# Kernel tuning notes

Measured on AMD Instinct MI355X. Metric: run time of the kernel, lower is better.

Reference implementation:

```python
import jax, jax.numpy as jnp
import numpy as np

TOK_DIM = 512
POS_DIM = 512
N_HEADS = 16
HEAD_DIM = 64
D_MODEL = 1024
INNER = N_HEADS * HEAD_DIM
B, T = 4, 2048


def setup_inputs() -> dict:
    key = jax.random.key(0)
    ks = jax.random.split(key, 5)
    s = 0.02
    return {
        "x": jax.random.normal(ks[0], (B, T, TOK_DIM + POS_DIM), dtype=jnp.float32),
        "Wq": jax.random.normal(ks[1], (POS_DIM, INNER), dtype=jnp.float32) * s,
        "Wk": jax.random.normal(ks[2], (POS_DIM, INNER), dtype=jnp.float32) * s,
        "Wv": jax.random.normal(ks[3], (TOK_DIM, INNER), dtype=jnp.float32) * s,
        "Wo": jax.random.normal(ks[4], (INNER, D_MODEL), dtype=jnp.float32) * s,
    }


def reference(x, Wq, Wk, Wv, Wo):
    b, t, _ = x.shape
    x_tok = x[:, :, :TOK_DIM]
    x_pos = x[:, :, TOK_DIM:]
    # project and split heads: [B, H, T, Dh]
    q = (x_pos @ Wq).reshape(b, t, N_HEADS, HEAD_DIM).transpose(0, 2, 1, 3)
    k = (x_pos @ Wk).reshape(b, t, N_HEADS, HEAD_DIM).transpose(0, 2, 1, 3)
    v = (x_tok @ Wv).reshape(b, t, N_HEADS, HEAD_DIM).transpose(0, 2, 1, 3)
    att = jnp.einsum("bhqd,bhkd->bhqk", q, k) / jnp.sqrt(jnp.float32(HEAD_DIM))
    causal = jnp.tril(jnp.ones((t, t), dtype=bool))
    att = jnp.where(causal, att, -jnp.inf)
    att = jax.nn.softmax(att, axis=-1)
    out = jnp.einsum("bhqk,bhkd->bhqd", att, v)
    out = out.transpose(0, 2, 1, 3).reshape(b, t, INNER)
    return out @ Wo
```

## Files before the change

kernel.cpp:

```cpp
#include <hip/hip_runtime.h>
#include <stdint.h>


typedef unsigned short u16;
typedef __bf16 bf16;
typedef bf16 bf16x8 __attribute__((ext_vector_type(8)));
typedef u16 u16x8 __attribute__((ext_vector_type(8)));
typedef u16 u16x4 __attribute__((ext_vector_type(4)));
typedef float f32x4 __attribute__((ext_vector_type(4)));
typedef uint32_t u32x4 __attribute__((ext_vector_type(4)));

__device__ __forceinline__ u16 cvt_bf16(float f) {
  uint32_t u = __builtin_bit_cast(uint32_t, f);
  u += 0x7FFFu + ((u >> 16) & 1u);
  return (u16)(u >> 16);
}

__device__ __forceinline__ f32x4 mfma_bf(bf16x8 a, bf16x8 b, f32x4 c) {
  return __builtin_amdgcn_mfma_f32_16x16x32_bf16(a, b, c, 0, 0, 0);
}

typedef __attribute__((address_space(1))) const uint32_t g_u32;
typedef __attribute__((address_space(3))) uint32_t l_u32;
__device__ __forceinline__ void gload16(const u16* g, u16* l) {
  __builtin_amdgcn_global_load_lds((g_u32*)g, (l_u32*)l, 16, 0, 0);
}

__global__ __launch_bounds__(256) void prep(
    const float* __restrict__ x, const float* __restrict__ Wq,
    const float* __restrict__ Wk, const float* __restrict__ Wv,
    const float* __restrict__ Wo, u16* __restrict__ xtok,
    u16* __restrict__ xpos, u16* __restrict__ Wt, u16* __restrict__ WoT) {
  const int gid = blockIdx.x;
  const int tid = threadIdx.x;
  if (gid < 1024) {
    const int z = gid >> 8;
    const float* src = (z == 0) ? Wq : (z == 1) ? Wk : (z == 2) ? Wv : Wo;
    const int K = (z == 3) ? 1024 : 512;
    u16* dst = (z == 3) ? WoT : (Wt + (size_t)z * 1024 * 512);
    const int k0 = ((gid >> 4) & 15) * 64, n0 = (gid & 15) * 64;
    if (k0 >= K) return;
    __shared__ u16 T[64][68];
    const int r = tid >> 4, c = (tid & 15) * 4;
#pragma unroll
    for (int i = 0; i < 4; i++) {
      float4 v = *(const float4*)(src + (size_t)(k0 + r + i * 16) * 1024 + n0 + c);
      u16x4 b = {cvt_bf16(v.x), cvt_bf16(v.y), cvt_bf16(v.z), cvt_bf16(v.w)};
      *(u16x4*)&T[r + i * 16][c] = b;
    }
    __syncthreads();
#pragma unroll
    for (int i = 0; i < 4; i++) {
      int n = r + i * 16;
      u16x4 v;
#pragma unroll
      for (int j = 0; j < 4; j++) v[j] = T[c + j][n];
      *(u16x4*)(dst + (size_t)(n0 + n) * K + k0 + c) = v;
    }
  } else {
    int idx = (gid - 1024) * 256 + tid;
    int row = idx >> 8;
    int c4 = (idx & 255) * 4;
    float4 v = *(const float4*)(x + (size_t)row * 1024 + c4);
    u16x4 b = {cvt_bf16(v.x), cvt_bf16(v.y), cvt_bf16(v.z), cvt_bf16(v.w)};
    u16* dst = (c4 < 512) ? (xtok + (size_t)row * 512 + c4)
                          : (xpos + (size_t)row * 512 + c4 - 512);
    *(u16x4*)dst = b;
  }
}


#define YLD(P) {                                                             \
  const u16* pa_ = rA + (P)*4096;                                            \
  af[0] = *(const bf16x8*)(pa_ + 0*512 + colx);                              \
  af[1] = *(const bf16x8*)(pa_ + 1*512 + colx);                              \
  af[2] = *(const bf16x8*)(pa_ + 2*512 + colx);                              \
  af[3] = *(const bf16x8*)(pa_ + 3*512 + colx);                              \
  const u16* pb_ = rB + (P)*4096;                                            \
  bf[0] = *(const bf16x8*)(pb_ + 0*512 + colx);                              \
  bf[1] = *(const bf16x8*)(pb_ + 1*512 + colx);                              \
  bf[2] = *(const bf16x8*)(pb_ + 2*512 + colx);                              \
  bf[3] = *(const bf16x8*)(pb_ + 3*512 + colx); }

#define YMM {                                                                \
  acc[0][0] = mfma_bf(af[0], bf[0], acc[0][0]);                              \
  acc[0][1] = mfma_bf(af[0], bf[1], acc[0][1]);                              \
  acc[0][2] = mfma_bf(af[0], bf[2], acc[0][2]);                              \
  acc[0][3] = mfma_bf(af[0], bf[3], acc[0][3]);                              \
  acc[1][0] = mfma_bf(af[1], bf[0], acc[1][0]);                              \
  acc[1][1] = mfma_bf(af[1], bf[1], acc[1][1]);                              \
  acc[1][2] = mfma_bf(af[1], bf[2], acc[1][2]);                              \
  acc[1][3] = mfma_bf(af[1], bf[3], acc[1][3]);                              \
  acc[2][0] = mfma_bf(af[2], bf[0], acc[2][0]);                              \
  acc[2][1] = mfma_bf(af[2], bf[1], acc[2][1]);                              \
  acc[2][2] = mfma_bf(af[2], bf[2], acc[2][2]);                              \
  acc[2][3] = mfma_bf(af[2], bf[3], acc[2][3]);                              \
  acc[3][0] = mfma_bf(af[3], bf[0], acc[3][0]);                              \
  acc[3][1] = mfma_bf(af[3], bf[1], acc[3][1]);                              \
  acc[3][2] = mfma_bf(af[3], bf[2], acc[3][2]);                              \
  acc[3][3] = mfma_bf(af[3], bf[3], acc[3][3]); }

#define YST(P, KT) {                                                         \
  gload16(gA + (KT)*32, lA + (P)*4096);                                      \
  gload16(gA + (size_t)64*Kd + (KT)*32, lA + (P)*4096 + 2048);               \
  gload16(gB + (KT)*32, lB + (P)*4096);                                      \
  gload16(gB + (size_t)64*Kd + (KT)*32, lB + (P)*4096 + 2048); }

#define YPH_MID  asm volatile("" ::: "memory"); __builtin_amdgcn_s_barrier();\
  asm volatile("s_waitcnt lgkmcnt(0)" ::: "memory");                         \
  __builtin_amdgcn_s_setprio(1);

#define YPH_END  __builtin_amdgcn_s_setprio(0);                              \
  asm volatile("s_waitcnt vmcnt(4)" ::: "memory");                           \
  asm volatile("" ::: "memory"); __builtin_amdgcn_s_barrier();

template <int Kd>
__device__ __forceinline__ void gemm128_core(
    const u16* __restrict__ Aptr, const u16* __restrict__ Bptr,
    int m0, int n0, u16* smem, f32x4 (&acc)[4][4]) {
  constexpr int NKT = Kd / 32;
  const int tid = threadIdx.x;
  const int lane = tid & 63;
  const int mrow = lane & 15, quad = lane >> 4;
  const int w = tid >> 6, wm = w >> 1, wn = w & 1;

  u16* As = smem;
  u16* Bs = smem + 12288;

  const int lrs = tid >> 2, sp4 = tid & 3;
  const int slog = sp4 ^ (lrs & 3);
  const u16* gA = Aptr + (size_t)(m0 + lrs) * Kd + slog * 8;
  const u16* gB = Bptr + (size_t)(n0 + lrs) * Kd + slog * 8;
  u16* lA = As + tid * 8;
  u16* lB = Bs + tid * 8;

  const int colx = ((quad ^ (mrow & 3)) * 8);
  const u16* rA = As + (wm * 64 + mrow) * 32;
  const u16* rB = Bs + (wn * 64 + mrow) * 32;

  bf16x8 af[4], bf[4];

  YST(0, 0) YST(1, 1)
  asm volatile("s_waitcnt vmcnt(4)" ::: "memory");
  asm volatile("" ::: "memory");
  __builtin_amdgcn_s_barrier();

  int p = 0, ps = 2;
  for (int t = 0; t < NKT; ++t) {
    const int kt = (t + 2 < NKT) ? t + 2 : NKT - 1;
    YLD(p)
    YST(ps, kt)
    YPH_MID
    YMM
    YPH_END
    p = (p == 2) ? 0 : p + 1;
    ps = (ps == 2) ? 0 : ps + 1;
  }
  asm volatile("s_waitcnt vmcnt(0)" ::: "memory");
  __builtin_amdgcn_s_barrier();
}

__device__ __forceinline__ void xcd_remap(int& bx, int& by) {
  int flat = blockIdx.x + 8 * blockIdx.y;
  int wg = (flat & 7) * 64 + (flat >> 3);
  bx = wg & 7;
  by = wg >> 3;
}

__global__ __launch_bounds__(256, 3) void gemm_qkv128(
    const u16* __restrict__ xtok, const u16* __restrict__ xpos,
    const u16* __restrict__ Wt, u16* __restrict__ qkv,
    u16* __restrict__ vperm) {
  const int z = blockIdx.z;
  const u16* A = (z == 2) ? xtok : xpos;
  const u16* Bt = Wt + (size_t)z * 1024 * 512;
  u16* outp = qkv + (size_t)z * (64u * 2048u * 64u);
  const float osc = (z == 0) ? 0.18033688011112042f : 1.0f;
  int bx, by;
  xcd_remap(bx, by);
  const int m0 = by * 128, n0 = bx * 128;

  __shared__ __align__(16) u16 smem[24576];
  f32x4 acc[4][4];
#pragma unroll
  for (int i = 0; i < 4; i++)
#pragma unroll
    for (int j = 0; j < 4; j++) acc[i][j] = (f32x4){0.f, 0.f, 0.f, 0.f};

  gemm128_core<512>(A, Bt, m0, n0, smem, acc);

  const int tid = threadIdx.x;
  const int lane = tid & 63;
  const int mrow = lane & 15, quad = lane >> 4;
  const int w = tid >> 6, wm = w >> 1, wn = w & 1;

  if (z != 2) {
#pragma unroll
    for (int mi = 0; mi < 4; mi++)
#pragma unroll
      for (int ni = 0; ni < 4; ni++)
#pragma unroll
        for (int r = 0; r < 4; r++) {
          int m = m0 + wm * 64 + mi * 16 + quad * 4 + r;
          int n = n0 + wn * 64 + ni * 16 + mrow;
          int bb = m >> 11, t = m & 2047;
          int h = n >> 6, d = n & 63;
          outp[(((size_t)(bb * 16 + h)) * 2048 + t) * 64 + d] =
              cvt_bf16(acc[mi][ni][r] * osc);
        }
  } else {
#pragma unroll
    for (int mi = 0; mi < 4; mi++)
#pragma unroll
      for (int ni = 0; ni < 4; ni++)
#pragma unroll
        for (int r = 0; r < 4; r++) {
          int m = m0 + wm * 64 + mi * 16 + quad * 4 + r;
          int n = n0 + wn * 64 + ni * 16 + mrow;
          int bb = m >> 11, t = m & 2047;
          int h = n >> 6, d = n & 63;
          int k6 = t & 63;
          int pos = (k6 & 32) + ((k6 >> 4) & 1) * 4 + ((k6 >> 2) & 3) * 8 +
                    (k6 & 3);
          vperm[(((size_t)(bb * 16 + h)) * 64 + d) * 2048 + (t & ~63) + pos] =
              cvt_bf16(acc[mi][ni][r]);
        }
  }
}

__global__ __launch_bounds__(256, 3) void gemm_out128(
    const u16* __restrict__ Am, const u16* __restrict__ WoT,
    float* __restrict__ out) {
  int bx, by;
  xcd_remap(bx, by);
  const int m0 = by * 128, n0 = bx * 128;

  __shared__ __align__(16) u16 smem[24576];
  f32x4 acc[4][4];
#pragma unroll
  for (int i = 0; i < 4; i++)
#pragma unroll
    for (int j = 0; j < 4; j++) acc[i][j] = (f32x4){0.f, 0.f, 0.f, 0.f};

  gemm128_core<1024>(Am, WoT, m0, n0, smem, acc);

  const int tid = threadIdx.x;
  const int lane = tid & 63;
  const int mrow = lane & 15, quad = lane >> 4;
  const int w = tid >> 6, wm = w >> 1, wn = w & 1;

#pragma unroll
  for (int mi = 0; mi < 4; mi++)
#pragma unroll
    for (int ni = 0; ni < 4; ni++)
#pragma unroll
      for (int r = 0; r < 4; r++) {
        int m = m0 + wm * 64 + mi * 16 + quad * 4 + r;
        int n = n0 + wn * 64 + ni * 16 + mrow;
        out[(size_t)m * 1024 + n] = acc[mi][ni][r];
      }
}

__global__ __launch_bounds__(256, 3) void attn(
    const u16* __restrict__ qkv, const u16* __restrict__ vperm,
    u16* __restrict__ aout) {
  const int bh = blockIdx.x;
  const int qt = 15 - blockIdx.y;
  const int bb = bh >> 4, h = bh & 15;
  const u16* Qp = qkv + (size_t)bh * (2048 * 64);
  const u16* Kp = qkv + (size_t)(64 + bh) * (2048 * 64);
  const u16* Vp = vperm + (size_t)bh * (64 * 2048);

  __shared__ __align__(16) u16 smem[2][4][64 * 32];

  const int tid = threadIdx.x;
  const int lane = tid & 63;
  const int w = tid >> 6;
  const int mrow = lane & 15;
  const int quad = lane >> 4;
  const int srow = w * 16 + (lane >> 2);
  const int sc = (lane & 3) * 8;
  const int soff = srow * 32 + sc;

  const u16x8 onesu = {0x3F80, 0x3F80, 0x3F80, 0x3F80,
                       0x3F80, 0x3F80, 0x3F80, 0x3F80};
  const bf16x8 ones = __builtin_bit_cast(bf16x8, onesu);

  const u16* kgb = Kp + (size_t)srow * 64 + sc;
  const u16* vgb = Vp + (size_t)srow * 2048 + sc;

  const int q0 = qt * 128;
  const int nk = 2 * qt + 2;
  const int qw = q0 + w * 32;

  const u16* qbase = Qp + (size_t)(qw + mrow) * 64 + quad * 8;
  const bf16x8 qf00 = *(const bf16x8*)qbase;
  const bf16x8 qf01 = *(const bf16x8*)(qbase + 32);
  const bf16x8 qf10 = *(const bf16x8*)(qbase + 16 * 64);
  const bf16x8 qf11 = *(const bf16x8*)(qbase + 16 * 64 + 32);

  f32x4 o[2][4], ol[2];
#pragma unroll
  for (int g = 0; g < 2; ++g) {
#pragma unroll
    for (int dt = 0; dt < 4; ++dt) o[g][dt] = (f32x4){0.f, 0.f, 0.f, 0.f};
    ol[g] = (f32x4){0.f, 0.f, 0.f, 0.f};
  }

  u16x8 ka0 = *(const u16x8*)kgb;
  u16x8 ka1 = *(const u16x8*)(kgb + 32);
  u16x8 va0 = *(const u16x8*)vgb;
  u16x8 va1 = *(const u16x8*)(vgb + 32);

  for (int it = 0; it < nk; ++it) {
    u16* buf = &smem[it & 1][0][0];
    *(u16x8*)(buf + 0 * 2048 + soff) = ka0;
    *(u16x8*)(buf + 1 * 2048 + soff) = ka1;
    *(u16x8*)(buf + 2 * 2048 + soff) = va0;
    *(u16x8*)(buf + 3 * 2048 + soff) = va1;

    if (it + 1 < nk) {
      const int kn = (it + 1) * 64;
      ka0 = *(const u16x8*)(kgb + (size_t)kn * 64);
      ka1 = *(const u16x8*)(kgb + (size_t)kn * 64 + 32);
      va0 = *(const u16x8*)(vgb + kn);
      va1 = *(const u16x8*)(vgb + kn + 32);
    }

    __syncthreads();

    const int k0 = it * 64;
    if (k0 > qw + 31) continue;

    f32x4 s[2][4];
#pragma unroll
    for (int nt = 0; nt < 4; ++nt) {
      bf16x8 kf0 = *(const bf16x8*)(buf + 0 * 2048 + (nt * 16 + mrow) * 32 + quad * 8);
      bf16x8 kf1 = *(const bf16x8*)(buf + 1 * 2048 + (nt * 16 + mrow) * 32 + quad * 8);
      f32x4 z0 = (f32x4){0.f, 0.f, 0.f, 0.f};
      z0 = mfma_bf(kf0, qf00, z0);
      s[0][nt] = mfma_bf(kf1, qf01, z0);
      f32x4 z1 = (f32x4){0.f, 0.f, 0.f, 0.f};
      z1 = mfma_bf(kf0, qf10, z1);
      s[1][nt] = mfma_bf(kf1, qf11, z1);
    }

    if (k0 + 63 > qw) {
#pragma unroll
      for (int g = 0; g < 2; ++g)
#pragma unroll
        for (int nt = 0; nt < 4; ++nt)
#pragma unroll
          for (int r = 0; r < 4; ++r)
            if (k0 + nt * 16 + quad * 4 + r > qw + g * 16 + mrow)
              s[g][nt][r] = -1e30f;
    }
#pragma unroll
    for (int g = 0; g < 2; ++g)
#pragma unroll
      for (int nt = 0; nt < 4; ++nt)
#pragma unroll
        for (int r = 0; r < 4; ++r)
          s[g][nt][r] = __builtin_amdgcn_exp2f(s[g][nt][r]);

    bf16x8 pf[2][2];
#pragma unroll
    for (int g = 0; g < 2; ++g) {
      pf[g][0] = (bf16x8){(bf16)s[g][0][0], (bf16)s[g][0][1],
                          (bf16)s[g][0][2], (bf16)s[g][0][3],
                          (bf16)s[g][1][0], (bf16)s[g][1][1],
                          (bf16)s[g][1][2], (bf16)s[g][1][3]};
      pf[g][1] = (bf16x8){(bf16)s[g][2][0], (bf16)s[g][2][1],
                          (bf16)s[g][2][2], (bf16)s[g][2][3],
                          (bf16)s[g][3][0], (bf16)s[g][3][1],
                          (bf16)s[g][3][2], (bf16)s[g][3][3]};
      ol[g] = mfma_bf(ones, pf[g][0], ol[g]);
      ol[g] = mfma_bf(ones, pf[g][1], ol[g]);
    }

#pragma unroll
    for (int dt = 0; dt < 4; ++dt) {
      bf16x8 vf0 = *(const bf16x8*)(buf + 2 * 2048 + (dt * 16 + mrow) * 32 + quad * 8);
      bf16x8 vf1 = *(const bf16x8*)(buf + 3 * 2048 + (dt * 16 + mrow) * 32 + quad * 8);
      o[0][dt] = mfma_bf(vf0, pf[0][0], o[0][dt]);
      o[0][dt] = mfma_bf(vf1, pf[0][1], o[0][dt]);
      o[1][dt] = mfma_bf(vf0, pf[1][0], o[1][dt]);
      o[1][dt] = mfma_bf(vf1, pf[1][1], o[1][dt]);
    }
  }

  __syncthreads();
  u16* Osh = &smem[0][0][0];

#pragma unroll
  for (int g = 0; g < 2; ++g) {
    const float inv = 1.f / ol[g][0];
#pragma unroll
    for (int dt = 0; dt < 4; ++dt)
#pragma unroll
      for (int r = 0; r < 4; ++r)
        Osh[(w * 32 + g * 16 + mrow) * 72 + dt * 16 + quad * 4 + r] =
            cvt_bf16(o[g][dt][r] * inv);
  }
#pragma unroll
  for (int p = 0; p < 4; ++p) {
    int ql = (lane >> 3) + 8 * p;
    int ch = lane & 7;
    u16x8 v = *(const u16x8*)&Osh[(w * 32 + ql) * 72 + ch * 8];
    int t = q0 + w * 32 + ql;
    *(u16x8*)(aout + ((size_t)(bb * 2048 + t)) * 1024 + h * 64 + ch * 8) = v;
  }
}

extern "C" void kernel_launch(void* const* d_in, const int* in_sizes, int n_in,
                              void* d_out, int out_size, void* d_ws, size_t ws_size,
                              hipStream_t stream) {
  const float* x  = (const float*)d_in[0];
  const float* Wq = (const float*)d_in[1];
  const float* Wk = (const float*)d_in[2];
  const float* Wv = (const float*)d_in[3];
  const float* Wo = (const float*)d_in[4];

  u16* qkv   = (u16*)d_ws;
  u16* vperm = qkv + (size_t)3 * 64 * 2048 * 64;
  u16* aout  = vperm + (size_t)64 * 64 * 2048;
  u16* xtok  = aout + (size_t)8192 * 1024;
  u16* xpos  = xtok + (size_t)8192 * 512;
  u16* Wt    = xpos + (size_t)8192 * 512;
  u16* WoT   = Wt + (size_t)3 * 1024 * 512;
  float* out = (float*)d_out;

  prep<<<dim3(1024 + 8192), dim3(256), 0, stream>>>(x, Wq, Wk, Wv, Wo, xtok,
                                                    xpos, Wt, WoT);
  gemm_qkv128<<<dim3(8, 64, 3), dim3(256), 0, stream>>>(xtok, xpos, Wt, qkv, vperm);
  attn<<<dim3(64, 16), dim3(256), 0, stream>>>(qkv, vperm, aout);
  gemm_out128<<<dim3(8, 64), dim3(256), 0, stream>>>(aout, WoT, out);
}
```

Before: 189.1 us.

## Software-pipeline attention loop: overlap PV of previous tile with QK of current

Restructures the attention inner loop so the P·V MFMAs for the previous key tile are issued after the current tile's QK^T MFMAs and before its exp/convert. This lets the independent matrix work cover the latency of the softmax and conversions. V tiles now use a triple buffer in shared memory, so the previous tile's V stays valid across the barrier. Shared memory grows from 16K to 20K u16 elements, which may lower occupancy, and the extra live P fragments raise register pressure.

```diff
diff --git a/kernel.cpp b/kernel.cpp
--- a/kernel.cpp
+++ b/kernel.cpp
@@ -271,7 +271,9 @@
   const u16* Kp = qkv + (size_t)(64 + bh) * (2048 * 64);
   const u16* Vp = vperm + (size_t)bh * (64 * 2048);
 
-  __shared__ __align__(16) u16 smem[2][4][64 * 32];
+  __shared__ __align__(16) u16 smem[20480];
+  u16* Ks = smem;
+  u16* Vs = smem + 8192;
 
   const int tid = threadIdx.x;
   const int lane = tid & 63;
@@ -300,11 +302,14 @@
   const bf16x8 qf11 = *(const bf16x8*)(qbase + 16 * 64 + 32);
 
   f32x4 o[2][4], ol[2];
+  bf16x8 pfp[2][2];
 #pragma unroll
   for (int g = 0; g < 2; ++g) {
 #pragma unroll
     for (int dt = 0; dt < 4; ++dt) o[g][dt] = (f32x4){0.f, 0.f, 0.f, 0.f};
     ol[g] = (f32x4){0.f, 0.f, 0.f, 0.f};
+    pfp[g][0] = __builtin_bit_cast(bf16x8, (u16x8){0,0,0,0,0,0,0,0});
+    pfp[g][1] = pfp[g][0];
   }
 
   u16x8 ka0 = *(const u16x8*)kgb;
@@ -312,12 +317,16 @@
   u16x8 va0 = *(const u16x8*)vgb;
   u16x8 va1 = *(const u16x8*)(vgb + 32);
 
+  int vb = 0;
+  const u16* vbPrev = Vs;
+
   for (int it = 0; it < nk; ++it) {
-    u16* buf = &smem[it & 1][0][0];
-    *(u16x8*)(buf + 0 * 2048 + soff) = ka0;
-    *(u16x8*)(buf + 1 * 2048 + soff) = ka1;
-    *(u16x8*)(buf + 2 * 2048 + soff) = va0;
-    *(u16x8*)(buf + 3 * 2048 + soff) = va1;
+    u16* kw = Ks + (it & 1) * 4096;
+    u16* vw = Vs + vb * 4096;
+    *(u16x8*)(kw + soff) = ka0;
+    *(u16x8*)(kw + 2048 + soff) = ka1;
+    *(u16x8*)(vw + soff) = va0;
+    *(u16x8*)(vw + 2048 + soff) = va1;
 
     if (it + 1 < nk) {
       const int kn = (it + 1) * 64;
@@ -330,67 +339,91 @@
     __syncthreads();
 
     const int k0 = it * 64;
-    if (k0 > qw + 31) continue;
+    const bool doQK = (k0 <= qw + 31);
 
     f32x4 s[2][4];
-#pragma unroll
-    for (int nt = 0; nt < 4; ++nt) {
-      bf16x8 kf0 = *(const bf16x8*)(buf + 0 * 2048 + (nt * 16 + mrow) * 32 + quad * 8);
-      bf16x8 kf1 = *(const bf16x8*)(buf + 1 * 2048 + (nt * 16 + mrow) * 32 + quad * 8);
-      f32x4 z0 = (f32x4){0.f, 0.f, 0.f, 0.f};
-      z0 = mfma_bf(kf0, qf00, z0);
-      s[0][nt] = mfma_bf(kf1, qf01, z0);
-      f32x4 z1 = (f32x4){0.f, 0.f, 0.f, 0.f};
-      z1 = mfma_bf(kf0, qf10, z1);
-      s[1][nt] = mfma_bf(kf1, qf11, z1);
-    }
-
-    if (k0 + 63 > qw) {
+    if (doQK) {
+#pragma unroll
+      for (int nt = 0; nt < 4; ++nt) {
+        bf16x8 kf0 = *(const bf16x8*)(kw + (nt * 16 + mrow) * 32 + quad * 8);
+        bf16x8 kf1 =
+            *(const bf16x8*)(kw + 2048 + (nt * 16 + mrow) * 32 + quad * 8);
+        f32x4 z0 = (f32x4){0.f, 0.f, 0.f, 0.f};
+        z0 = mfma_bf(kf0, qf00, z0);
+        s[0][nt] = mfma_bf(kf1, qf01, z0);
+        f32x4 z1 = (f32x4){0.f, 0.f, 0.f, 0.f};
+        z1 = mfma_bf(kf0, qf10, z1);
+        s[1][nt] = mfma_bf(kf1, qf11, z1);
+      }
+    }
+
+    if (it > 0 && k0 - 64 <= qw + 31) {
+#pragma unroll
+      for (int dt = 0; dt < 4; ++dt) {
+        bf16x8 vf0 =
+            *(const bf16x8*)(vbPrev + (dt * 16 + mrow) * 32 + quad * 8);
+        bf16x8 vf1 =
+            *(const bf16x8*)(vbPrev + 2048 + (dt * 16 + mrow) * 32 + quad * 8);
+        o[0][dt] = mfma_bf(vf0, pfp[0][0], o[0][dt]);
+        o[0][dt] = mfma_bf(vf1, pfp[0][1], o[0][dt]);
+        o[1][dt] = mfma_bf(vf0, pfp[1][0], o[1][dt]);
+        o[1][dt] = mfma_bf(vf1, pfp[1][1], o[1][dt]);
+      }
+    }
+
+    if (doQK) {
+      if (k0 + 63 > qw) {
+#pragma unroll
+        for (int g = 0; g < 2; ++g)
+#pragma unroll
+          for (int nt = 0; nt < 4; ++nt)
+#pragma unroll
+            for (int r = 0; r < 4; ++r)
+              if (k0 + nt * 16 + quad * 4 + r > qw + g * 16 + mrow)
+                s[g][nt][r] = -1e30f;
+      }
 #pragma unroll
       for (int g = 0; g < 2; ++g)
 #pragma unroll
         for (int nt = 0; nt < 4; ++nt)
 #pragma unroll
           for (int r = 0; r < 4; ++r)
-            if (k0 + nt * 16 + quad * 4 + r > qw + g * 16 + mrow)
-              s[g][nt][r] = -1e30f;
-    }
-#pragma unroll
-    for (int g = 0; g < 2; ++g)
-#pragma unroll
-      for (int nt = 0; nt < 4; ++nt)
-#pragma unroll
-        for (int r = 0; r < 4; ++r)
-          s[g][nt][r] = __builtin_amdgcn_exp2f(s[g][nt][r]);
-
-    bf16x8 pf[2][2];
-#pragma unroll
-    for (int g = 0; g < 2; ++g) {
-      pf[g][0] = (bf16x8){(bf16)s[g][0][0], (bf16)s[g][0][1],
-                          (bf16)s[g][0][2], (bf16)s[g][0][3],
-                          (bf16)s[g][1][0], (bf16)s[g][1][1],
-                          (bf16)s[g][1][2], (bf16)s[g][1][3]};
-      pf[g][1] = (bf16x8){(bf16)s[g][2][0], (bf16)s[g][2][1],
-                          (bf16)s[g][2][2], (bf16)s[g][2][3],
-                          (bf16)s[g][3][0], (bf16)s[g][3][1],
-                          (bf16)s[g][3][2], (bf16)s[g][3][3]};
-      ol[g] = mfma_bf(ones, pf[g][0], ol[g]);
-      ol[g] = mfma_bf(ones, pf[g][1], ol[g]);
-    }
-
+            s[g][nt][r] = __builtin_amdgcn_exp2f(s[g][nt][r]);
+
+#pragma unroll
+      for (int g = 0; g < 2; ++g) {
+        pfp[g][0] = (bf16x8){(bf16)s[g][0][0], (bf16)s[g][0][1],
+                             (bf16)s[g][0][2], (bf16)s[g][0][3],
+                             (bf16)s[g][1][0], (bf16)s[g][1][1],
+                             (bf16)s[g][1][2], (bf16)s[g][1][3]};
+        pfp[g][1] = (bf16x8){(bf16)s[g][2][0], (bf16)s[g][2][1],
+                             (bf16)s[g][2][2], (bf16)s[g][2][3],
+                             (bf16)s[g][3][0], (bf16)s[g][3][1],
+                             (bf16)s[g][3][2], (bf16)s[g][3][3]};
+        ol[g] = mfma_bf(ones, pfp[g][0], ol[g]);
+        ol[g] = mfma_bf(ones, pfp[g][1], ol[g]);
+      }
+    }
+
+    vbPrev = vw;
+    vb = (vb == 2) ? 0 : vb + 1;
+  }
+
+  if ((nk - 1) * 64 <= qw + 31) {
 #pragma unroll
     for (int dt = 0; dt < 4; ++dt) {
-      bf16x8 vf0 = *(const bf16x8*)(buf + 2 * 2048 + (dt * 16 + mrow) * 32 + quad * 8);
-      bf16x8 vf1 = *(const bf16x8*)(buf + 3 * 2048 + (dt * 16 + mrow) * 32 + quad * 8);
-      o[0][dt] = mfma_bf(vf0, pf[0][0], o[0][dt]);
-      o[0][dt] = mfma_bf(vf1, pf[0][1], o[0][dt]);
-      o[1][dt] = mfma_bf(vf0, pf[1][0], o[1][dt]);
-      o[1][dt] = mfma_bf(vf1, pf[1][1], o[1][dt]);
+      bf16x8 vf0 = *(const bf16x8*)(vbPrev + (dt * 16 + mrow) * 32 + quad * 8);
+      bf16x8 vf1 =
+          *(const bf16x8*)(vbPrev + 2048 + (dt * 16 + mrow) * 32 + quad * 8);
+      o[0][dt] = mfma_bf(vf0, pfp[0][0], o[0][dt]);
+      o[0][dt] = mfma_bf(vf1, pfp[0][1], o[0][dt]);
+      o[1][dt] = mfma_bf(vf0, pfp[1][0], o[1][dt]);
+      o[1][dt] = mfma_bf(vf1, pfp[1][1], o[1][dt]);
     }
   }
 
   __syncthreads();
-  u16* Osh = &smem[0][0][0];
+  u16* Osh = smem;
 
 #pragma unroll
   for (int g = 0; g < 2; ++g) {
```

Result: no change. 189.8 us (+0.4%).
